# Performance work log

Hardware: AMD Instinct MI355X
Metric: run time of the kernel (lower is better)

## Reference

```python
import jax, jax.numpy as jnp
import numpy as np

B, H, W, C = 1, 64, 64, 768
NUM_HEADS = 12
HEAD_DIM = C // NUM_HEADS  # 64


def setup_inputs() -> dict:
    key = jax.random.key(0)
    ks = jax.random.split(key, 7)
    s = 0.02
    return {
        "imagelike_bhwc": jax.random.normal(ks[0], (B, H, W, C), dtype=jnp.float32),
        "qkv_w": jax.random.normal(ks[1], (C, 3 * C), dtype=jnp.float32) * s,
        "qkv_b": jax.random.normal(ks[2], (3 * C,), dtype=jnp.float32) * s,
        "proj_w": jax.random.normal(ks[3], (C, C), dtype=jnp.float32) * s,
        "proj_b": jax.random.normal(ks[4], (C,), dtype=jnp.float32) * s,
        "rel_pos_h": jax.random.normal(ks[5], (2 * H - 1, HEAD_DIM), dtype=jnp.float32) * s,
        "rel_pos_w": jax.random.normal(ks[6], (2 * W - 1, HEAD_DIM), dtype=jnp.float32) * s,
    }


def reference(imagelike_bhwc, qkv_w, qkv_b, proj_w, proj_b, rel_pos_h, rel_pos_w):
    b, h, w, c = imagelike_bhwc.shape
    n = h * w
    nh, hd = NUM_HEADS, c // NUM_HEADS
    scale = hd ** (-0.5)

    # qkv projection -> (3, B*nh, N, hd)
    qkv = imagelike_bhwc @ qkv_w + qkv_b  # (b,h,w,3c)
    qkv = qkv.reshape(b, n, 3, nh, hd).transpose(2, 0, 3, 1, 4).reshape(3, b * nh, n, hd)
    q, k, v = qkv[0], qkv[1], qkv[2]

    # scaled dot-product scores
    attn = jnp.einsum("bqd,bkd->bqk", q * scale, k)  # (b*nh, n, n)

    # decomposed relative position bias (query grid == key grid == base grid)
    idx_h = jnp.arange(h)[:, None] - jnp.arange(h)[None, :] + (h - 1)  # (h,h)
    idx_w = jnp.arange(w)[:, None] - jnp.arange(w)[None, :] + (w - 1)  # (w,w)
    Rh = rel_pos_h[idx_h]  # (h, h, hd)
    Rw = rel_pos_w[idx_w]  # (w, w, hd)
    r_q = q.reshape(b * nh, h, w, hd)
    rel_h = jnp.einsum("bhwc,hkc->bhwk", r_q, Rh)  # (b*nh, h, w, h)
    rel_w = jnp.einsum("bhwc,wkc->bhwk", r_q, Rw)  # (b*nh, h, w, w)
    bias = (rel_h[:, :, :, :, None] + rel_w[:, :, :, None, :]).reshape(b * nh, n, n)

    attn = jax.nn.softmax(attn + bias, axis=-1)
    out = jnp.einsum("bqk,bkd->bqd", attn, v)  # (b*nh, n, hd)

    out = out.reshape(b, nh, h, w, hd).transpose(0, 2, 3, 1, 4).reshape(b, h, w, c)
    return out @ proj_w + proj_b
```

## Files before the change

kernel.cpp:

```cpp
#include <hip/hip_runtime.h>
#include <stdint.h>

typedef unsigned short u16;
typedef __bf16 bf16x8 __attribute__((ext_vector_type(8)));
typedef float f32x4 __attribute__((ext_vector_type(4)));
typedef unsigned short ushort8 __attribute__((ext_vector_type(8)));
typedef unsigned short ushort4v __attribute__((ext_vector_type(4)));

#define MFMA __builtin_amdgcn_mfma_f32_16x16x32_bf16
#define EXP2 __builtin_amdgcn_exp2f

__device__ __forceinline__ u16 f2bf(float f){
  uint32_t u = __builtin_bit_cast(uint32_t, f);
  u += 0x7fffu + ((u >> 16) & 1u);
  return (u16)(u >> 16);
}
__device__ __forceinline__ float bf2f(u16 h){
  uint32_t u = ((uint32_t)h) << 16;
  return __builtin_bit_cast(float, u);
}
__device__ __forceinline__ uint32_t cvtpk(float lo, float hi){
  uint32_t r;
  asm("v_cvt_pk_bf16_f32 %0, %1, %2" : "=v"(r) : "v"(lo), "v"(hi));
  return r;
}
__device__ __forceinline__ bf16x8 ld8(const u16* p){
  return __builtin_bit_cast(bf16x8, *(const ushort8*)p);
}
__device__ __forceinline__ void gload16(const void* g, void* l){
  __builtin_amdgcn_global_load_lds((__attribute__((address_space(1))) void*)(void*)g,
                                   (__attribute__((address_space(3))) void*)l, 16, 0, 0);
}


__global__ __launch_bounds__(256) void k_conv8(const float* __restrict__ in, u16* __restrict__ out){
  int i = blockIdx.x*256 + threadIdx.x;
  const float4* p = (const float4*)in;
  float4 a = p[i*2], b = p[i*2+1];
  ushort8 o;
  o[0]=f2bf(a.x); o[1]=f2bf(a.y); o[2]=f2bf(a.z); o[3]=f2bf(a.w);
  o[4]=f2bf(b.x); o[5]=f2bf(b.y); o[6]=f2bf(b.z); o[7]=f2bf(b.w);
  ((ushort8*)out)[i] = o;
}

__global__ __launch_bounds__(256) void k_tr(const float* __restrict__ in, u16* __restrict__ out,
                                            int R, int Cc){
  __shared__ float tile[64][65];
  int r0 = blockIdx.x*64, c0 = blockIdx.y*64;
  int t = threadIdx.x;
  int c = t & 63, r4 = t >> 6;
  for (int i = 0; i < 16; ++i)
    tile[r4 + i*4][c] = in[(size_t)(r0 + r4 + i*4)*Cc + c0 + c];
  __syncthreads();
  for (int i = 0; i < 16; ++i){
    int rr = r4 + i*4;
    out[(size_t)(c0 + rr)*R + r0 + c] = f2bf(tile[c][rr]);
  }
}

__global__ __launch_bounds__(256) void k_relconv(const float* __restrict__ rh, const float* __restrict__ rw,
                                                 u16* __restrict__ rh8, u16* __restrict__ rw8){
  int i = blockIdx.x*256 + threadIdx.x;
  if (i < 8192)      rh8[i] = f2bf(i < 8128 ? rh[i]*8.0f : 0.0f);
  else { int j = i - 8192; rw8[j] = f2bf(j < 8128 ? rw[j]*8.0f : 0.0f); }
}


__global__ __launch_bounds__(256) void k_qkv(const u16* __restrict__ X, const u16* __restrict__ WT,
                                             const float* __restrict__ bias,
                                             u16* __restrict__ Qs, u16* __restrict__ Kf, u16* __restrict__ Vf){
  __shared__ __align__(16) u16 At[128*64];
  __shared__ __align__(16) u16 Bt[128*64];
  __shared__ __align__(16) u16 Tt[4][64*72];
  const int tid = threadIdx.x, lane = tid & 63, w = tid >> 6;
  const int m0 = blockIdx.x*128, n0 = blockIdx.y*128;
  const int wr = (w >> 1)*64, wc = (w & 1)*64;
  const int lr = lane & 15, lg = lane >> 4;
  const int srcRow = w*32 + (lane >> 3);
  const int srcK   = (lane & 7)*8;
  f32x4 acc[4][4] = {};
  for (int kt = 0; kt < 12; ++kt){
    const int kbase = kt*64;
    for (int s = 0; s < 4; ++s){
      gload16(X  + (size_t)(m0 + srcRow + s*8)*768 + kbase + srcK, At + (w*32 + s*8)*64);
      gload16(WT + (size_t)(n0 + srcRow + s*8)*768 + kbase + srcK, Bt + (w*32 + s*8)*64);
    }
    __syncthreads();
    bf16x8 af[2][4], bfr[2][4];
    for (int ks = 0; ks < 2; ++ks)
      for (int i = 0; i < 4; ++i){
        af[ks][i]  = ld8(At + (wr + i*16 + lr)*64 + ks*32 + lg*8);
        bfr[ks][i] = ld8(Bt + (wc + i*16 + lr)*64 + ks*32 + lg*8);
      }
    for (int ks = 0; ks < 2; ++ks)
      for (int mi = 0; mi < 4; ++mi)
        for (int ni = 0; ni < 4; ++ni)
          acc[mi][ni] = MFMA(af[ks][mi], bfr[ks][ni], acc[mi][ni], 0, 0, 0);
    __syncthreads();
  }
  const int colbase = n0 + wc;
  const int s3 = colbase / 768;
  const int hh = (colbase % 768) >> 6;
  const int rowbase = m0 + wr;
  if (s3 == 0){
    for (int mi = 0; mi < 4; ++mi)
      for (int ni = 0; ni < 4; ++ni){
        float bv = bias[colbase + ni*16 + lr];
        for (int r = 0; r < 4; ++r){
          int row = rowbase + mi*16 + lg*4 + r;
          Qs[((size_t)hh*4096 + row)*64 + ni*16 + lr] =
              f2bf((acc[mi][ni][r] + bv)*(0.125f*1.44269504f));
        }
      }
  } else {
    u16* T = Tt[w];
    for (int mi = 0; mi < 4; ++mi)
      for (int ni = 0; ni < 4; ++ni){
        float bv = bias[colbase + ni*16 + lr];
        for (int r = 0; r < 4; ++r){
          int row_l = mi*16 + lg*4 + r, col_l = ni*16 + lr;
          u16 v = f2bf(acc[mi][ni][r] + bv);
          if (s3 == 1) T[row_l*72 + col_l] = v;
          else         T[col_l*72 + row_l] = v;
        }
      }
    const int kb = rowbase >> 6;
    u16* dst = (s3 == 1 ? Kf : Vf) + ((size_t)hh*64 + kb)*4096 + lane*8;
    #pragma unroll
    for (int f = 0; f < 8; ++f){
      int a = f >> 1, ks = f & 1;
      *(ushort8*)&dst[f*512] = *(const ushort8*)&T[(a*16 + lr)*72 + ks*32 + lg*8];
    }
  }
}


__global__ __launch_bounds__(256) void k_rel(const u16* __restrict__ Qs, const u16* __restrict__ Rh8,
                                             const u16* __restrict__ Rw8,
                                             u16* __restrict__ relh, u16* __restrict__ relw){
  __shared__ __align__(16) u16 Ql[64*64];
  __shared__ __align__(16) u16 Rhl[64*64];
  __shared__ __align__(16) u16 Rwl[128*64];
  const int tid = threadIdx.x, lane = tid & 63, w = tid >> 6;
  const int qh = blockIdx.x, h = blockIdx.y;
  const int lr = lane & 15, lg = lane >> 4;
  for (int j = 0; j < 2; ++j){
    int ch = tid + 256*j;
    int row = ch >> 3, k8 = (ch & 7)*8;
    *(ushort8*)&Ql[row*64 + k8]  = *(const ushort8*)&Qs[((size_t)h*4096 + qh*64 + row)*64 + k8];
    *(ushort8*)&Rhl[row*64 + k8] = *(const ushort8*)&Rh8[(qh + row)*64 + k8];
  }
  for (int j = 0; j < 4; ++j){
    int ch = tid + 256*j;
    int row = ch >> 3, k8 = (ch & 7)*8;
    *(ushort8*)&Rwl[row*64 + k8] = *(const ushort8*)&Rw8[row*64 + k8];
  }
  __syncthreads();
  bf16x8 a[2];
  for (int ks = 0; ks < 2; ++ks) a[ks] = ld8(Ql + (w*16 + lr)*64 + ks*32 + lg*8);
  for (int ct = 0; ct < 4; ++ct){
    f32x4 c = {};
    for (int ks = 0; ks < 2; ++ks)
      c = MFMA(a[ks], ld8(Rhl + (ct*16 + lr)*64 + ks*32 + lg*8), c, 0, 0, 0);
    int kh = 63 - (ct*16 + lr);
    for (int r = 0; r < 4; ++r){
      int qw = w*16 + lg*4 + r;
      relh[((size_t)h*4096 + qh*64 + qw)*64 + kh] = f2bf(c[r]);
    }
  }
  for (int ct = 0; ct < 8; ++ct){
    f32x4 c = {};
    for (int ks = 0; ks < 2; ++ks)
      c = MFMA(a[ks], ld8(Rwl + (ct*16 + lr)*64 + ks*32 + lg*8), c, 0, 0, 0);
    int cc = ct*16 + lr;
    for (int r = 0; r < 4; ++r){
      int qw = w*16 + lg*4 + r;
      int kw = qw + 63 - cc;
      if (kw >= 0 && kw < 64)
        relw[((size_t)h*4096 + qh*64 + qw)*64 + kw] = f2bf(c[r]);
    }
  }
}


__global__ __launch_bounds__(256, 3) void k_flash(const u16* __restrict__ Qs, const u16* __restrict__ Kf,
                                                  const u16* __restrict__ Vf,
                                                  const u16* __restrict__ relh, const u16* __restrict__ relw,
                                                  u16* __restrict__ Ob){
  __shared__ __align__(16) u16 Kl[2][4096];
  __shared__ __align__(16) u16 Vl[2][4096];
  __shared__ __align__(16) char Psm[4][2048];
  const int tid = threadIdx.x, lane = tid & 63, w = tid >> 6;
  const int b = blockIdx.x;
  const int p = (b & 7)*96 + (b >> 3);
  const int h = p >> 6, qb = p & 63;
  const int lr = lane & 15, lg = lane >> 4;
  const size_t hq = (size_t)h*4096;
  const int q = qb*64 + w*16 + lr;
  char* Pb = Psm[w];
  const int swz = (lr & 7) << 4;

  const bf16x8 qf0 = ld8(Qs + (hq + q)*64 + lg*8);
  const bf16x8 qf1 = ld8(Qs + (hq + q)*64 + 32 + lg*8);
  float rwf[4][4];
  #pragma unroll
  for (int ct = 0; ct < 4; ++ct){
    ushort4v t = *(const ushort4v*)&relw[(hq + q)*64 + ct*16 + lg*4];
    #pragma unroll
    for (int r = 0; r < 4; ++r) rwf[ct][r] = bf2f(t[r]);
  }

  const u16* KfH = Kf + (size_t)h*262144;
  const u16* VfH = Vf + (size_t)h*262144;
  const u16* rhbase = relh + (hq + q)*64;

  float m = -1e30f, lsum = 0.f;
  f32x4 oacc[4] = {};

  auto stage = [&](int buf, int kb){
    const u16* ks = KfH + kb*4096 + w*1024 + lane*8;
    const u16* vs = VfH + kb*4096 + w*1024 + lane*8;
    gload16(ks,       &Kl[buf][w*1024]);
    gload16(ks + 512, &Kl[buf][w*1024 + 512]);
    gload16(vs,       &Vl[buf][w*1024]);
    gload16(vs + 512, &Vl[buf][w*1024 + 512]);
  };

#define ITERBODY(KB, BUF)                                                     \
  {                                                                           \
    const u16* KL = Kl[BUF] + lane*8;                                         \
    const u16* VL = Vl[BUF] + lane*8;                                         \
    const float rhv = bf2f(rhbase[KB]);                                       \
    f32x4 s[4];                                                               \
    _Pragma("unroll")                                                         \
    for (int ct = 0; ct < 4; ++ct){                                           \
      _Pragma("unroll")                                                       \
      for (int r = 0; r < 4; ++r) s[ct][r] = rhv + rwf[ct][r];                \
    }                                                                         \
    __builtin_amdgcn_s_setprio(1);                                            \
    _Pragma("unroll")                                                         \
    for (int ct = 0; ct < 4; ++ct){                                           \
      s[ct] = MFMA(ld8(KL + (ct*2)*512),   qf0, s[ct], 0, 0, 0);              \
      s[ct] = MFMA(ld8(KL + (ct*2+1)*512), qf1, s[ct], 0, 0, 0);              \
    }                                                                         \
    __builtin_amdgcn_s_setprio(0);                                            \
               \
    float pm0 = fmaxf(fmaxf(s[0][0], s[0][1]), fmaxf(fmaxf(s[0][2], s[0][3]), \
                      fmaxf(s[1][0], s[1][1])));                              \
    float pm1 = fmaxf(fmaxf(s[1][2], s[1][3]), fmaxf(fmaxf(s[2][0], s[2][1]), \
                      fmaxf(s[2][2], s[2][3])));                              \
    float pm2 = fmaxf(fmaxf(s[3][0], s[3][1]), fmaxf(s[3][2], s[3][3]));      \
    float pm = fmaxf(fmaxf(pm0, pm1), pm2);                                   \
             \
    if (__any(pm > m)){                                                       \
      pm = fmaxf(pm, __shfl_xor(pm, 16, 64));                                 \
      pm = fmaxf(pm, __shfl_xor(pm, 32, 64));                                 \
      const float nm = fmaxf(m, pm);                                          \
      const float corr = EXP2(m - nm);                                        \
      m = nm;                                                                 \
      lsum *= corr;                                                           \
      _Pragma("unroll")                                                       \
      for (int dt = 0; dt < 4; ++dt)                                          \
        _Pragma("unroll")                                                     \
        for (int r = 0; r < 4; ++r) oacc[dt][r] *= corr;                      \
    }                                                                         \
    float rs = 0.f;                                                           \
    _Pragma("unroll")                                                         \
    for (int ct = 0; ct < 4; ++ct){                                           \
      _Pragma("unroll")                                                       \
      for (int r = 0; r < 4; ++r){                                            \
        float p2 = EXP2(s[ct][r] - m);                                        \
        s[ct][r] = p2; rs += p2;                                              \
      }                                                                       \
    }                                                                         \
    lsum += rs;                           \
    _Pragma("unroll")                                                         \
    for (int ct = 0; ct < 4; ++ct){                                           \
      uint2 uv;                                                               \
      uv.x = cvtpk(s[ct][0], s[ct][1]);                                       \
      uv.y = cvtpk(s[ct][2], s[ct][3]);                                       \
      *(uint2*)(Pb + ((lr*128 + ct*32 + lg*8) ^ swz)) = uv;                   \
    }                                                                         \
    bf16x8 pa0 = __builtin_bit_cast(bf16x8, *(ushort8*)(Pb + ((lr*128      + lg*16) ^ swz))); \
    bf16x8 pa1 = __builtin_bit_cast(bf16x8, *(ushort8*)(Pb + ((lr*128 + 64 + lg*16) ^ swz))); \
    __builtin_amdgcn_s_setprio(1);                                            \
    _Pragma("unroll")                                                         \
    for (int dt = 0; dt < 4; ++dt){                                           \
      oacc[dt] = MFMA(ld8(VL + (dt*2)*512),   pa0, oacc[dt], 0, 0, 0);        \
      oacc[dt] = MFMA(ld8(VL + (dt*2+1)*512), pa1, oacc[dt], 0, 0, 0);        \
    }                                                                         \
    __builtin_amdgcn_s_setprio(0);                                            \
  }

  stage(0, 0);
  __syncthreads();
  for (int kb2 = 0; kb2 < 64; kb2 += 2){
    stage(1, (kb2 + 1) & 63);
    ITERBODY(kb2, 0)
    __syncthreads();
    stage(0, (kb2 + 2) & 63);
    ITERBODY(kb2 + 1, 1)
    __syncthreads();
  }
#undef ITERBODY

  lsum += __shfl_xor(lsum, 16, 64);
  lsum += __shfl_xor(lsum, 32, 64);
  const float inv = 1.0f / lsum;
  #pragma unroll
  for (int dt = 0; dt < 4; ++dt){
    ushort4v pk;
    #pragma unroll
    for (int r = 0; r < 4; ++r) pk[r] = f2bf(oacc[dt][r]*inv);
    *(ushort4v*)&Ob[(size_t)q*768 + h*64 + dt*16 + lg*4] = pk;
  }
}


__global__ __launch_bounds__(256) void k_proj(const u16* __restrict__ A, const u16* __restrict__ WT,
                                              const float* __restrict__ bias, float* __restrict__ out){
  __shared__ __align__(16) u16 At[128*64];
  __shared__ __align__(16) u16 Bt[128*64];
  const int tid = threadIdx.x, lane = tid & 63, w = tid >> 6;
  const int m0 = blockIdx.x*128, n0 = blockIdx.y*128;
  const int wr = (w >> 1)*64, wc = (w & 1)*64;
  const int lr = lane & 15, lg = lane >> 4;
  const int srcRow = w*32 + (lane >> 3);
  const int srcK   = (lane & 7)*8;
  f32x4 acc[4][4] = {};
  for (int kt = 0; kt < 12; ++kt){
    const int kbase = kt*64;
    for (int s = 0; s < 4; ++s){
      gload16(A  + (size_t)(m0 + srcRow + s*8)*768 + kbase + srcK, At + (w*32 + s*8)*64);
      gload16(WT + (size_t)(n0 + srcRow + s*8)*768 + kbase + srcK, Bt + (w*32 + s*8)*64);
    }
    __syncthreads();
    bf16x8 af[2][4], bfr[2][4];
    for (int ks = 0; ks < 2; ++ks)
      for (int i = 0; i < 4; ++i){
        af[ks][i]  = ld8(At + (wr + i*16 + lr)*64 + ks*32 + lg*8);
        bfr[ks][i] = ld8(Bt + (wc + i*16 + lr)*64 + ks*32 + lg*8);
      }
    for (int ks = 0; ks < 2; ++ks)
      for (int mi = 0; mi < 4; ++mi)
        for (int ni = 0; ni < 4; ++ni)
          acc[mi][ni] = MFMA(af[ks][mi], bfr[ks][ni], acc[mi][ni], 0, 0, 0);
    __syncthreads();
  }
  for (int mi = 0; mi < 4; ++mi)
    for (int ni = 0; ni < 4; ++ni){
      int col = n0 + wc + ni*16 + lr;
      float bv = bias[col];
      for (int r = 0; r < 4; ++r){
        int row = m0 + wr + mi*16 + lg*4 + r;
        out[(size_t)row*768 + col] = acc[mi][ni][r] + bv;
      }
    }
}


extern "C" void kernel_launch(void* const* d_in, const int* in_sizes, int n_in,
                              void* d_out, int out_size, void* d_ws, size_t ws_size,
                              hipStream_t stream){
  const float* X32   = (const float*)d_in[0];
  const float* qkvw  = (const float*)d_in[1];
  const float* qkvb  = (const float*)d_in[2];
  const float* projw = (const float*)d_in[3];
  const float* projb = (const float*)d_in[4];
  const float* rposh = (const float*)d_in[5];
  const float* rposw = (const float*)d_in[6];

  u16* Xb  = (u16*)d_ws;
  u16* W1T = Xb  + 3145728;
  u16* PT  = W1T + 1769472;
  u16* Rh8 = PT  + 589824;
  u16* Rw8 = Rh8 + 8192;
  u16* Qs  = Rw8 + 8192;
  u16* Kf  = Qs  + 3145728;
  u16* Vf  = Kf  + 3145728;
  u16* Rlh = Vf  + 3145728;
  u16* Rlw = Rlh + 3145728;
  u16* Ob  = Rlw + 3145728;
  float* out = (float*)d_out;

  k_conv8  <<<1536, 256, 0, stream>>>(X32, Xb);
  k_tr     <<<dim3(12, 36), 256, 0, stream>>>(qkvw, W1T, 768, 2304);
  k_tr     <<<dim3(12, 12), 256, 0, stream>>>(projw, PT, 768, 768);
  k_relconv<<<64, 256, 0, stream>>>(rposh, rposw, Rh8, Rw8);
  k_qkv    <<<dim3(32, 18), 256, 0, stream>>>(Xb, W1T, qkvb, Qs, Kf, Vf);
  k_rel    <<<dim3(64, 12), 256, 0, stream>>>(Qs, Rh8, Rw8, Rlh, Rlw);
  k_flash  <<<768, 256, 0, stream>>>(Qs, Kf, Vf, Rlh, Rlw, Ob);
  k_proj   <<<dim3(32, 6), 256, 0, stream>>>(Ob, PT, projb, out);
}
```

Measured before the change: 176.8 us.

## Load K directly into registers in flash kernel and merge prep kernels

Replaces LDS staging of K tiles in the attention kernel with direct per-lane global loads into double-buffered register arrays, because each wave's K fragments map one-to-one onto its own lanes. This removes half the LDS footprint and the LDS reads for K, at the cost of more VGPRs under a 3-blocks-per-CU launch bound and global-load latency that is now exposed to the MFMA schedule. Separately, the four small preprocessing kernels (input conversion, two weight transposes, rel-pos conversion) are fused into one launch to cut launch overhead.

```diff
diff --git a/kernel.cpp b/kernel.cpp
--- a/kernel.cpp
+++ b/kernel.cpp
@@ -33,36 +33,48 @@
 }
 
 
-__global__ __launch_bounds__(256) void k_conv8(const float* __restrict__ in, u16* __restrict__ out){
-  int i = blockIdx.x*256 + threadIdx.x;
-  const float4* p = (const float4*)in;
-  float4 a = p[i*2], b = p[i*2+1];
-  ushort8 o;
-  o[0]=f2bf(a.x); o[1]=f2bf(a.y); o[2]=f2bf(a.z); o[3]=f2bf(a.w);
-  o[4]=f2bf(b.x); o[5]=f2bf(b.y); o[6]=f2bf(b.z); o[7]=f2bf(b.w);
-  ((ushort8*)out)[i] = o;
-}
-
-__global__ __launch_bounds__(256) void k_tr(const float* __restrict__ in, u16* __restrict__ out,
-                                            int R, int Cc){
-  __shared__ float tile[64][65];
-  int r0 = blockIdx.x*64, c0 = blockIdx.y*64;
-  int t = threadIdx.x;
+__device__ __forceinline__ void tr_body(const float* __restrict__ in, u16* __restrict__ out,
+                                        int R, int Cc, int bx, int by, int t, float* tile ){
+  int r0 = bx*64, c0 = by*64;
   int c = t & 63, r4 = t >> 6;
   for (int i = 0; i < 16; ++i)
-    tile[r4 + i*4][c] = in[(size_t)(r0 + r4 + i*4)*Cc + c0 + c];
+    tile[(r4 + i*4)*65 + c] = in[(size_t)(r0 + r4 + i*4)*Cc + c0 + c];
   __syncthreads();
   for (int i = 0; i < 16; ++i){
     int rr = r4 + i*4;
-    out[(size_t)(c0 + rr)*R + r0 + c] = f2bf(tile[c][rr]);
-  }
-}
-
-__global__ __launch_bounds__(256) void k_relconv(const float* __restrict__ rh, const float* __restrict__ rw,
-                                                 u16* __restrict__ rh8, u16* __restrict__ rw8){
-  int i = blockIdx.x*256 + threadIdx.x;
-  if (i < 8192)      rh8[i] = f2bf(i < 8128 ? rh[i]*8.0f : 0.0f);
-  else { int j = i - 8192; rw8[j] = f2bf(j < 8128 ? rw[j]*8.0f : 0.0f); }
+    out[(size_t)(c0 + rr)*R + r0 + c] = f2bf(tile[c*65 + rr]);
+  }
+}
+
+__global__ __launch_bounds__(256) void k_prep(const float* __restrict__ X32,
+                                              const float* __restrict__ qkvw,
+                                              const float* __restrict__ projw,
+                                              const float* __restrict__ rposh,
+                                              const float* __restrict__ rposw,
+                                              u16* __restrict__ Xb, u16* __restrict__ W1T,
+                                              u16* __restrict__ PT,
+                                              u16* __restrict__ rh8, u16* __restrict__ rw8){
+  __shared__ float tile[64*65];
+  const int b = blockIdx.x, t = threadIdx.x;
+  if (b < 1536){
+    int i = b*256 + t;
+    const float4* p = (const float4*)X32;
+    float4 a = p[i*2], c = p[i*2+1];
+    ushort8 o;
+    o[0]=f2bf(a.x); o[1]=f2bf(a.y); o[2]=f2bf(a.z); o[3]=f2bf(a.w);
+    o[4]=f2bf(c.x); o[5]=f2bf(c.y); o[6]=f2bf(c.z); o[7]=f2bf(c.w);
+    ((ushort8*)Xb)[i] = o;
+  } else if (b < 1968){
+    int bb = b - 1536;
+    tr_body(qkvw, W1T, 768, 2304, bb % 12, bb / 12, t, tile);
+  } else if (b < 2112){
+    int bb = b - 1968;
+    tr_body(projw, PT, 768, 768, bb % 12, bb / 12, t, tile);
+  } else {
+    int i = (b - 2112)*256 + t;
+    if (i < 8192)      rh8[i] = f2bf(i < 8128 ? rposh[i]*8.0f : 0.0f);
+    else { int j = i - 8192; rw8[j] = f2bf(j < 8128 ? rposw[j]*8.0f : 0.0f); }
+  }
 }
 
 
@@ -187,7 +199,6 @@
                                                   const u16* __restrict__ Vf,
                                                   const u16* __restrict__ relh, const u16* __restrict__ relw,
                                                   u16* __restrict__ Ob){
-  __shared__ __align__(16) u16 Kl[2][4096];
   __shared__ __align__(16) u16 Vl[2][4096];
   __shared__ __align__(16) char Psm[4][2048];
   const int tid = threadIdx.x, lane = tid & 63, w = tid >> 6;
@@ -210,25 +221,27 @@
     for (int r = 0; r < 4; ++r) rwf[ct][r] = bf2f(t[r]);
   }
 
-  const u16* KfH = Kf + (size_t)h*262144;
+  const u16* KfH = Kf + (size_t)h*262144 + lane*8;
   const u16* VfH = Vf + (size_t)h*262144;
   const u16* rhbase = relh + (hq + q)*64;
 
   float m = -1e30f, lsum = 0.f;
   f32x4 oacc[4] = {};
-
-  auto stage = [&](int buf, int kb){
-    const u16* ks = KfH + kb*4096 + w*1024 + lane*8;
+  bf16x8 kA[8], kB[8];
+
+  auto loadK = [&](bf16x8 (&dst)[8], int kbi){
+    const u16* kp = KfH + kbi*4096;
+    #pragma unroll
+    for (int f = 0; f < 8; ++f) dst[f] = ld8(kp + f*512);
+  };
+  auto stageV = [&](int buf, int kb){
     const u16* vs = VfH + kb*4096 + w*1024 + lane*8;
-    gload16(ks,       &Kl[buf][w*1024]);
-    gload16(ks + 512, &Kl[buf][w*1024 + 512]);
     gload16(vs,       &Vl[buf][w*1024]);
     gload16(vs + 512, &Vl[buf][w*1024 + 512]);
   };
 
-#define ITERBODY(KB, BUF)                                                     \
+#define ITERBODY(KB, KC, BUF)                                                 \
   {                                                                           \
-    const u16* KL = Kl[BUF] + lane*8;                                         \
     const u16* VL = Vl[BUF] + lane*8;                                         \
     const float rhv = bf2f(rhbase[KB]);                                       \
     f32x4 s[4];                                                               \
@@ -240,11 +253,11 @@
     __builtin_amdgcn_s_setprio(1);                                            \
     _Pragma("unroll")                                                         \
     for (int ct = 0; ct < 4; ++ct){                                           \
-      s[ct] = MFMA(ld8(KL + (ct*2)*512),   qf0, s[ct], 0, 0, 0);              \
-      s[ct] = MFMA(ld8(KL + (ct*2+1)*512), qf1, s[ct], 0, 0, 0);              \
+      s[ct] = MFMA(KC[ct*2],   qf0, s[ct], 0, 0, 0);                          \
+      s[ct] = MFMA(KC[ct*2+1], qf1, s[ct], 0, 0, 0);                          \
     }                                                                         \
     __builtin_amdgcn_s_setprio(0);                                            \
-               \
+                                       \
     float pm0 = fmaxf(fmaxf(s[0][0], s[0][1]), fmaxf(fmaxf(s[0][2], s[0][3]), \
                       fmaxf(s[1][0], s[1][1])));                              \
     float pm1 = fmaxf(fmaxf(s[1][2], s[1][3]), fmaxf(fmaxf(s[2][0], s[2][1]), \
@@ -292,14 +305,17 @@
     __builtin_amdgcn_s_setprio(0);                                            \
   }
 
-  stage(0, 0);
+  loadK(kA, 0);
+  stageV(0, 0);
   __syncthreads();
   for (int kb2 = 0; kb2 < 64; kb2 += 2){
-    stage(1, (kb2 + 1) & 63);
-    ITERBODY(kb2, 0)
-    __syncthreads();
-    stage(0, (kb2 + 2) & 63);
-    ITERBODY(kb2 + 1, 1)
+    stageV(1, (kb2 + 1) & 63);
+    loadK(kB, (kb2 + 1) & 63);
+    ITERBODY(kb2, kA, 0)
+    __syncthreads();
+    stageV(0, (kb2 + 2) & 63);
+    loadK(kA, (kb2 + 2) & 63);
+    ITERBODY(kb2 + 1, kB, 1)
     __syncthreads();
   }
 #undef ITERBODY
@@ -383,12 +399,9 @@
   u16* Ob  = Rlw + 3145728;
   float* out = (float*)d_out;
 
-  k_conv8  <<<1536, 256, 0, stream>>>(X32, Xb);
-  k_tr     <<<dim3(12, 36), 256, 0, stream>>>(qkvw, W1T, 768, 2304);
-  k_tr     <<<dim3(12, 12), 256, 0, stream>>>(projw, PT, 768, 768);
-  k_relconv<<<64, 256, 0, stream>>>(rposh, rposw, Rh8, Rw8);
-  k_qkv    <<<dim3(32, 18), 256, 0, stream>>>(Xb, W1T, qkvb, Qs, Kf, Vf);
-  k_rel    <<<dim3(64, 12), 256, 0, stream>>>(Qs, Rh8, Rw8, Rlh, Rlw);
-  k_flash  <<<768, 256, 0, stream>>>(Qs, Kf, Vf, Rlh, Rlw, Ob);
-  k_proj   <<<dim3(32, 6), 256, 0, stream>>>(Ob, PT, projb, out);
-}
+  k_prep <<<2176, 256, 0, stream>>>(X32, qkvw, projw, rposh, rposw, Xb, W1T, PT, Rh8, Rw8);
+  k_qkv  <<<dim3(32, 18), 256, 0, stream>>>(Xb, W1T, qkvb, Qs, Kf, Vf);
+  k_rel  <<<dim3(64, 12), 256, 0, stream>>>(Qs, Rh8, Rw8, Rlh, Rlw);
+  k_flash<<<768, 256, 0, stream>>>(Qs, Kf, Vf, Rlh, Rlw, Ob);
+  k_proj <<<dim3(32, 6), 256, 0, stream>>>(Ob, PT, projb, out);
+}
```

Measured after the change: 179.6 us. About the same (+1.6%).
